# Kernel tuning notes

Measured on AMD Instinct MI355X. Metric: run time of the kernel, lower is better.

Reference implementation:

```python
import jax, jax.numpy as jnp
import numpy as np

NEG = -1e30  # safe 'log zero' for fp32 (avoids -inf NaNs in grads)


def _ctc_loss(logits, targets, input_lengths, target_lengths):
    """PyTorch-semantics CTC loss: blank=0, reduction='mean', zero_infinity=True.
    logits: [B,T,C] (pre-log-softmax), targets: [B,S] padded, lengths: [B].
    """
    B, T, C = logits.shape
    S = targets.shape[1]
    L = 2 * S + 1  # extended target length (blanks interleaved)
    logp = jax.nn.log_softmax(logits, axis=-1)  # [B,T,C]

    # extended targets: blank, y1, blank, y2, ..., blank
    ext = jnp.zeros((B, L), jnp.int32).at[:, 1::2].set(targets.astype(jnp.int32))
    lp_ext = jnp.take_along_axis(
        logp, jnp.broadcast_to(ext[:, None, :], (B, T, L)), axis=2)  # [B,T,L]

    pos = jnp.arange(L)
    ext_m2 = jnp.pad(ext, ((0, 0), (2, 0)))[:, :L]
    can_skip = (ext != 0) & (ext != ext_m2) & (pos >= 2)  # [B,L]

    def shift(a, k):
        return jnp.pad(a, ((0, 0), (k, 0)), constant_values=NEG)[:, :L]

    def lse3(a, b, c):
        m = jnp.maximum(jnp.maximum(a, b), c)
        return m + jnp.log(jnp.exp(a - m) + jnp.exp(b - m) + jnp.exp(c - m))

    alpha0 = (jnp.full((B, L), NEG, logits.dtype)
              .at[:, 0].set(lp_ext[:, 0, 0])
              .at[:, 1].set(lp_ext[:, 0, 1]))

    def step(alpha, xs):
        lp_t, t = xs  # lp_t: [B,L]
        a2 = shift(alpha, 1)
        a3 = jnp.where(can_skip, shift(alpha, 2), NEG)
        new = lp_t + lse3(alpha, a2, a3)
        # freeze alpha once past each sample's input_length
        alpha = jnp.where((t < input_lengths)[:, None], new, alpha)
        return alpha, None

    lp_T = jnp.swapaxes(lp_ext, 0, 1)  # [T,B,L]
    alpha, _ = jax.lax.scan(step, alpha0, (lp_T[1:], jnp.arange(1, T)))

    i1 = (2 * target_lengths - 1).astype(jnp.int32)
    i2 = (2 * target_lengths).astype(jnp.int32)
    a_last = jnp.take_along_axis(alpha, i1[:, None], axis=1)[:, 0]
    a_blank = jnp.take_along_axis(alpha, i2[:, None], axis=1)[:, 0]
    loss = -jnp.logaddexp(a_last, a_blank)  # [B]
    loss = jnp.where(loss > 1e29, 0.0, loss)  # zero_infinity=True
    return jnp.mean(loss / target_lengths.astype(loss.dtype))


def setup_inputs() -> dict:
    key = jax.random.key(0)
    ks = jax.random.split(key, 8)
    B, T = 32, 2000
    C_err, S_err = 4, 50
    C_ph, S_ph = 64, 200
    error_logits = jax.random.normal(ks[0], (B, T, C_err), jnp.float32)
    phoneme_logits = jax.random.normal(ks[1], (B, T, C_ph), jnp.float32)
    # labels in [1, C): blank=0 never appears in targets
    error_targets = jax.random.randint(ks[2], (B, S_err), 1, C_err, jnp.int32)
    phoneme_targets = jax.random.randint(ks[3], (B, S_ph), 1, C_ph, jnp.int32)
    error_input_lengths = jax.random.randint(ks[4], (B,), T - T // 4, T + 1, jnp.int32)
    phoneme_input_lengths = jax.random.randint(ks[5], (B,), T - T // 4, T + 1, jnp.int32)
    error_target_lengths = jax.random.randint(ks[6], (B,), S_err // 2, S_err + 1, jnp.int32)
    phoneme_target_lengths = jax.random.randint(ks[7], (B,), S_ph // 2, S_ph + 1, jnp.int32)
    return {
        "error_logits": error_logits,
        "phoneme_logits": phoneme_logits,
        "error_targets": error_targets,
        "phoneme_targets": phoneme_targets,
        "error_input_lengths": error_input_lengths,
        "phoneme_input_lengths": phoneme_input_lengths,
        "error_target_lengths": error_target_lengths,
        "phoneme_target_lengths": phoneme_target_lengths,
    }


def reference(error_logits, phoneme_logits, error_targets, phoneme_targets,
              error_input_lengths, phoneme_input_lengths,
              error_target_lengths, phoneme_target_lengths):
    error_weight = 1.0
    phoneme_weight = 1.0
    error_loss = _ctc_loss(error_logits, error_targets,
                           error_input_lengths, error_target_lengths)
    phoneme_loss = _ctc_loss(phoneme_logits, phoneme_targets,
                             phoneme_input_lengths, phoneme_target_lengths)
    total_loss = error_weight * error_loss + phoneme_weight * phoneme_loss
    return total_loss
```

## Files before the change

kernel.cpp:

```cpp
#include <hip/hip_runtime.h>
#include <math.h>


static constexpr float  LOG2E = 1.4426950408889634f;
static constexpr double LN2D  = 0.6931471805599453;
static constexpr int GROWS = 2032;

#define DPP_WAVE_SHR1   0x138
#define DPP_ROW_SHR(n)  (0x110 | (n))
#define DPP_ROW_BCAST15 0x142
#define DPP_ROW_BCAST31 0x143

__device__ __forceinline__ float fexp2(float x) {
  return __builtin_amdgcn_exp2f(x);
}
__device__ __forceinline__ float flog2(float x) {
  return __builtin_amdgcn_logf(x);
}

__device__ __forceinline__ double dpp_shr1_f64(double x) {
  int lo = __double2loint(x), hi = __double2hiint(x);
  lo = __builtin_amdgcn_update_dpp(0, lo, DPP_WAVE_SHR1, 0xf, 0xf, true);
  hi = __builtin_amdgcn_update_dpp(0, hi, DPP_WAVE_SHR1, 0xf, 0xf, true);
  return __hiloint2double(hi, lo);
}

__device__ __forceinline__ int imax2(int a, int b) { return a > b ? a : b; }

__device__ __forceinline__ int wave_imax(int v) {
  v = imax2(v, __builtin_amdgcn_update_dpp(0, v, DPP_ROW_SHR(1), 0xf, 0xf, true));
  v = imax2(v, __builtin_amdgcn_update_dpp(0, v, DPP_ROW_SHR(2), 0xf, 0xf, true));
  v = imax2(v, __builtin_amdgcn_update_dpp(0, v, DPP_ROW_SHR(4), 0xf, 0xf, true));
  v = imax2(v, __builtin_amdgcn_update_dpp(0, v, DPP_ROW_SHR(8), 0xf, 0xf, true));
  v = imax2(v, __builtin_amdgcn_update_dpp(0, v, DPP_ROW_BCAST15, 0xf, 0xf, true));
  v = imax2(v, __builtin_amdgcn_update_dpp(0, v, DPP_ROW_BCAST31, 0xf, 0xf, true));
  return __builtin_amdgcn_readlane(v, 63);
}

template <int SZ>
__device__ __forceinline__ void dma(const float* g, float* l) {
  auto gp = (const __attribute__((address_space(1))) void*)g;
  auto lp = (__attribute__((address_space(3))) void*)l;
  if constexpr (SZ == 4) {
    __builtin_amdgcn_global_load_lds(gp, lp, 4, 0, 0);
  } else {
    __builtin_amdgcn_global_load_lds(gp, lp, 16, 0, 0);
  }
}

__device__ __forceinline__ void wait_vmcnt16() {
  __builtin_amdgcn_sched_barrier(0);
  __builtin_amdgcn_s_waitcnt(20336);
  __builtin_amdgcn_sched_barrier(0);
}
__device__ __forceinline__ void wait_vmcnt0() {
  __builtin_amdgcn_sched_barrier(0);
  __builtin_amdgcn_s_waitcnt(3952);
  __builtin_amdgcn_sched_barrier(0);
}


__global__ __launch_bounds__(256) void gather_all_kernel(
    const float* __restrict__ ph_logits, const float* __restrict__ err_logits,
    const int* __restrict__ ph_tgt, const int* __restrict__ err_tgt,
    float* __restrict__ Gph, float* __restrict__ Ger,
    float* __restrict__ Lpb_ph, float* __restrict__ Lpb_er) {
  const int lane = threadIdx.x & 63;
  const int t = blockIdx.x * 4 + (threadIdx.x >> 6);
  const int b = blockIdx.y;
  if (blockIdx.z == 0) {
    const float z = ph_logits[((size_t)b * 2000 + t) * 64 + lane] * LOG2E;
    float m = z;
#pragma unroll
    for (int off = 32; off >= 1; off >>= 1) m = fmaxf(m, __shfl_xor(m, off, 64));
    const float zm = z - m;
    const float e = fexp2(zm);
    float s = e;
#pragma unroll
    for (int off = 32; off >= 1; off >>= 1) s += __shfl_xor(s, off, 64);
    const int ei = __float_as_int(e);
    const float e0 = __int_as_float(__builtin_amdgcn_readlane(ei, 0));
    const float inv0 = 1.0f / e0;
    const int* tb = ph_tgt + b * 200;
    float o[4];
#pragma unroll
    for (int k = 0; k < 4; ++k) {
      const int si = lane * 4 + k;
      const int cls = (si < 200) ? tb[si] : 0;
      const float v = __int_as_float(__builtin_amdgcn_ds_bpermute(cls << 2, ei));
      o[k] = (si < 200) ? (v * inv0) : 0.0f;
    }
    *(float4*)(Gph + ((size_t)b * GROWS + t) * 256 + lane * 4) =
        make_float4(o[0], o[1], o[2], o[3]);
    if (lane == 0)
      Lpb_ph[(size_t)b * GROWS + t] = zm - flog2(s);
  } else {
    const float4 v = *(const float4*)(err_logits + ((size_t)b * 2000 + t) * 4);
    const float z0 = v.x * LOG2E, z1 = v.y * LOG2E, z2 = v.z * LOG2E,
                z3 = v.w * LOG2E;
    const float m = fmaxf(fmaxf(z0, z1), fmaxf(z2, z3));
    const float e0 = fexp2(z0 - m), e1 = fexp2(z1 - m);
    const float e2 = fexp2(z2 - m), e3 = fexp2(z3 - m);
    const int c1 = err_tgt[b * 50 + (lane < 50 ? lane : 49)];
    const float num = (c1 == 1) ? e1 : (c1 == 2) ? e2 : e3;
    Ger[((size_t)b * GROWS + t) * 64 + lane] = (lane < 50) ? (num / e0) : 0.0f;
    if (lane == 0)
      Lpb_er[(size_t)b * GROWS + t] = (z0 - m) - flog2(e0 + e1 + e2 + e3);
  }
}

template <int P> struct RowP { float v[P]; };

template <int P>
__device__ __forceinline__ RowP<P> load_rowp(const float* p) {
  RowP<P> r;
  if constexpr (P == 4) {
    const float4 a = *(const float4*)p;
    r.v[0] = a.x; r.v[1] = a.y; r.v[2] = a.z; r.v[3] = a.w;
  } else {
    r.v[0] = *p;
  }
  return r;
}

template <int P>
__device__ __forceinline__ void bl_renorm(double (&B)[P], double (&L)[P],
                                          int& K) {
  double mm = B[0];
#pragma unroll
  for (int k = 0; k < P; ++k) mm = fmax(fmax(mm, B[k]), L[k]);
  const int ex = (__double2hiint(mm) >> 20) & 0x7ff;
  const int emax = wave_imax(ex);
  if (emax > 0) {
    int d = 1523 - emax;
    if (d > 1023) d = 1023;
    if (d < -1022) d = -1022;
    const double sc = __hiloint2double((d + 1023) << 20, 0);
#pragma unroll
    for (int k = 0; k < P; ++k) { B[k] *= sc; L[k] *= sc; }
    K += d;
  }
}

template <int P>
__device__ __forceinline__ void bl_step(double (&B)[P], double (&L)[P],
                                        const double (&skipm)[P],
                                        const RowP<P>& f) {
  const double Lm1 = dpp_shr1_f64(L[P - 1]);
  double nB[P], nL[P];
#pragma unroll
  for (int k = 0; k < P; ++k) {
    const double Lp = (k >= 1) ? L[k - 1] : Lm1;
    nB[k] = B[k] + Lp;
    nL[k] = (double)f.v[k] * fma(skipm[k], Lp, B[k] + L[k]);
  }
#pragma unroll
  for (int k = 0; k < P; ++k) { B[k] = nB[k]; L[k] = nL[k]; }
}

template <int P, int S>
__device__ __forceinline__ void chain_bl3(
    const float* __restrict__ Glab,
    const float* __restrict__ Lpb,
    const int* __restrict__ tb, int len, int tl,
    float* __restrict__ out, double* sa, float* stage) {
  constexpr int LSTRIDE = 64 * P;
  const int lane = threadIdx.x;

  float spb = 0.f;
  for (int t = lane; t < len; t += 64) spb += Lpb[t];
#pragma unroll
  for (int off = 32; off >= 1; off >>= 1) spb += __shfl_xor(spb, off, 64);

  double skipm[P];
#pragma unroll
  for (int k = 0; k < P; ++k) {
    const int s = lane * P + k;
    skipm[k] = (s >= 1 && s < S && tb[s] != tb[s - 1]) ? 1.0 : 0.0;
  }

  double B[P], L[P];
#pragma unroll
  for (int k = 0; k < P; ++k) { B[k] = 0.0; L[k] = 0.0; }
  {
    const float r0 = Glab[0];
    if (lane == 0) { B[0] = 1.0; L[0] = (double)r0; }
  }
  int K = 0;

  const int ngroups = (len - 1) / 16;
  auto issue_group = [&](int g, int buf) {
    const float* rb = Glab + (size_t)(1 + g * 16) * LSTRIDE + lane * P;
    float* lb = stage + (size_t)buf * 16 * LSTRIDE;
#pragma unroll
    for (int u = 0; u < 16; ++u)
      dma<P * 4>(rb + u * LSTRIDE, lb + u * LSTRIDE);
  };

  if (ngroups >= 1) issue_group(0, 0);
  if (ngroups >= 2) issue_group(1, 1);

  for (int g = 0; g < ngroups; ++g) {
    if (g + 1 < ngroups) wait_vmcnt16();
    else                 wait_vmcnt0();
    bl_renorm<P>(B, L, K);
    const float* lb = stage + (size_t)(g & 1) * 16 * LSTRIDE + lane * P;
    RowP<P> c0 = load_rowp<P>(lb);
    RowP<P> c1 = load_rowp<P>(lb + LSTRIDE);
#pragma unroll
    for (int u = 0; u < 16; ++u) {
      RowP<P> c2 = c1;
      if (u + 2 < 16) c2 = load_rowp<P>(lb + (u + 2) * LSTRIDE);
      bl_step<P>(B, L, skipm, c0);
      c0 = c1; c1 = c2;
    }
    if (g + 2 < ngroups) issue_group(g + 2, g & 1);
  }
  for (int t = 1 + ngroups * 16; t < len; ++t) {
    if (((t - 1) & 15) == 0) bl_renorm<P>(B, L, K);
    const RowP<P> f = load_rowp<P>(Glab + (size_t)t * LSTRIDE + lane * P);
    bl_step<P>(B, L, skipm, f);
  }

  double* saB = sa;
  double* saL = sa + 64 * P;
#pragma unroll
  for (int k = 0; k < P; ++k) {
    saB[lane * P + k] = B[k];
    saL[lane * P + k] = L[k];
  }
  __syncthreads();
  if (lane == 0) {
    const double a = saL[tl - 1] + saB[tl];
    float loss = (float)((double)K * LN2D - log(a) - (double)spb * LN2D);
    if (!(loss < 1e29f)) loss = 0.f;
    atomicAdd(out, loss / ((float)tl * 32.0f));
  }
}

__global__ __launch_bounds__(64) void ctc_chains_dma_kernel(
    const float* __restrict__ Gph, const float* __restrict__ Ger,
    const float* __restrict__ Lpb_ph, const float* __restrict__ Lpb_er,
    const int* __restrict__ err_tgt, const int* __restrict__ ph_tgt,
    const int* __restrict__ err_il, const int* __restrict__ ph_il,
    const int* __restrict__ err_tl, const int* __restrict__ ph_tl,
    float* __restrict__ out) {
  __shared__ float stage[2 * 16 * 256];
  __shared__ double sa[512];
  const int blk = blockIdx.x;
  if (blk < 32) {
    int len = err_il[blk]; if (len > 2000) len = 2000;
    chain_bl3<1, 50>(Ger + (size_t)blk * GROWS * 64,
                     Lpb_er + (size_t)blk * GROWS, err_tgt + blk * 50, len,
                     err_tl[blk], out, sa, stage);
  } else {
    const int b = blk - 32;
    int len = ph_il[b]; if (len > 2000) len = 2000;
    chain_bl3<4, 200>(Gph + (size_t)b * GROWS * 256,
                      Lpb_ph + (size_t)b * GROWS, ph_tgt + b * 200, len,
                      ph_tl[b], out, sa, stage);
  }
}


__global__ __launch_bounds__(256) void softmax4_kernel(
    const float* __restrict__ x, float* __restrict__ p, int nrows) {
  int r = blockIdx.x * blockDim.x + threadIdx.x;
  if (r >= nrows) return;
  float4 v = *reinterpret_cast<const float4*>(x + (size_t)r * 4);
  float z0 = v.x * LOG2E, z1 = v.y * LOG2E, z2 = v.z * LOG2E, z3 = v.w * LOG2E;
  float m = fmaxf(fmaxf(z0, z1), fmaxf(z2, z3));
  float e0 = fexp2(z0 - m), e1 = fexp2(z1 - m);
  float e2 = fexp2(z2 - m), e3 = fexp2(z3 - m);
  float inv = 1.0f / (e0 + e1 + e2 + e3);
  float4 o;
  o.x = e0 * inv; o.y = e1 * inv; o.z = e2 * inv; o.w = e3 * inv;
  *reinterpret_cast<float4*>(p + (size_t)r * 4) = o;
}

__global__ __launch_bounds__(256) void softmax64_kernel(
    const float* __restrict__ x, float* __restrict__ p, int nrows) {
  int row = blockIdx.x * 4 + (threadIdx.x >> 6);
  int lane = threadIdx.x & 63;
  if (row >= nrows) return;
  float z = x[(size_t)row * 64 + lane] * LOG2E;
  float m = z;
#pragma unroll
  for (int off = 32; off >= 1; off >>= 1) m = fmaxf(m, __shfl_xor(m, off, 64));
  float e = fexp2(z - m);
  float s = e;
#pragma unroll
  for (int off = 32; off >= 1; off >>= 1) s += __shfl_xor(s, off, 64);
  p[(size_t)row * 64 + lane] = e * (1.0f / s);
}

template <int C, int S, int R>
__device__ __forceinline__ void ctc_chain_lin_fb(
    const float* __restrict__ p_b, const int* __restrict__ tgt_b,
    int len, int tl, float* __restrict__ out, double* sa) {
  constexpr int L = 2 * S + 1;
  const int lane = threadIdx.x;
  int idx[R];
  double skipm[R];
#pragma unroll
  for (int j = 0; j < R; ++j) {
    const int l = lane * R + j;
    int cls = 0;
    bool sk = false;
    if (l & 1) {
      const int s = (l - 1) >> 1;
      const int sc = (s < S) ? s : (S - 1);
      cls = tgt_b[sc];
      if (s >= 1 && s < S) sk = (cls != tgt_b[s - 1]);
    }
    idx[j] = cls * 4;
    skipm[j] = sk ? 1.0 : 0.0;
  }
  double alpha[R];
#pragma unroll
  for (int j = 0; j < R; ++j) {
    const int l = lane * R + j;
    alpha[j] = (l <= 1) ? (double)p_b[idx[j] >> 2] : 0.0;
  }
  int K = 0;
  const int cl = lane & (C - 1);
  float rv = p_b[(size_t)((1 < len - 1) ? 1 : (len - 1)) * C + cl];
  float pf[R];
#pragma unroll
  for (int j = 0; j < R; ++j)
    pf[j] = __int_as_float(__builtin_amdgcn_ds_bpermute(idx[j], __float_as_int(rv)));
  rv = p_b[(size_t)((2 < len - 1) ? 2 : (len - 1)) * C + cl];
  for (int t = 1; t < len; ++t) {
    if ((t & 31) == 0) {
      double m = alpha[0];
#pragma unroll
      for (int j = 1; j < R; ++j) m = fmax(m, alpha[j]);
#pragma unroll
      for (int off = 1; off < 64; off <<= 1) m = fmax(m, __shfl_xor(m, off, 64));
      const long long bits = __double_as_longlong(m);
      const int e = (int)((bits >> 52) & 0x7FF);
      if (e > 0) {
        const double sc = __longlong_as_double((long long)(2046 - e) << 52);
#pragma unroll
        for (int j = 0; j < R; ++j) alpha[j] *= sc;
        K += 1023 - e;
      }
    }
    const int tn = (t + 2 < len) ? (t + 2) : (len - 1);
    const float rvn = p_b[(size_t)tn * C + cl];
    float pfn[R];
#pragma unroll
    for (int j = 0; j < R; ++j)
      pfn[j] = __int_as_float(__builtin_amdgcn_ds_bpermute(idx[j], __float_as_int(rv)));
    double am1 = __shfl_up(alpha[R - 1], 1, 64);
    double am2 = __shfl_up(alpha[R - 2], 1, 64);
    if (lane == 0) { am1 = 0.0; am2 = 0.0; }
    double na[R];
#pragma unroll
    for (int j = 0; j < R; ++j) {
      const double a0 = alpha[j];
      const double a1 = (j >= 1) ? alpha[j - 1] : am1;
      const double a2 = (j >= 2) ? alpha[j - 2] : ((j == 1) ? am1 : am2);
      double s = a0 + a1;
      s = fma(skipm[j], a2, s);
      na[j] = (double)pf[j] * s;
    }
#pragma unroll
    for (int j = 0; j < R; ++j) alpha[j] = na[j];
#pragma unroll
    for (int j = 0; j < R; ++j) pf[j] = pfn[j];
    rv = rvn;
  }
#pragma unroll
  for (int j = 0; j < R; ++j) {
    const int l = lane * R + j;
    if (l < L) sa[l] = alpha[j];
  }
  __syncthreads();
  if (lane == 0) {
    const double a = sa[2 * tl - 1] + sa[2 * tl];
    float loss = (float)((double)K * LN2D - log(a));
    if (!(loss < 1e29f)) loss = 0.0f;
    atomicAdd(out, loss / ((float)tl * 32.0f));
  }
}

__global__ __launch_bounds__(64) void ctc_chains_fb_kernel(
    const float* __restrict__ p_err, const float* __restrict__ p_ph,
    const int* __restrict__ err_tgt, const int* __restrict__ ph_tgt,
    const int* __restrict__ err_il, const int* __restrict__ ph_il,
    const int* __restrict__ err_tl, const int* __restrict__ ph_tl,
    float* __restrict__ out) {
  __shared__ double sa[512];
  const int T = 2000;
  const int blk = blockIdx.x;
  if (blk < 32) {
    const int b = blk;
    int len = err_il[b]; if (len > T) len = T;
    ctc_chain_lin_fb<4, 50, 2>(p_err + (size_t)b * T * 4, err_tgt + b * 50, len,
                               err_tl[b], out, sa);
  } else {
    const int b = blk - 32;
    int len = ph_il[b]; if (len > T) len = T;
    ctc_chain_lin_fb<64, 200, 7>(p_ph + (size_t)b * T * 64, ph_tgt + b * 200,
                                 len, ph_tl[b], out, sa);
  }
}


extern "C" void kernel_launch(void* const* d_in, const int* in_sizes, int n_in,
                              void* d_out, int out_size, void* d_ws,
                              size_t ws_size, hipStream_t stream) {
  const float* err_logits = (const float*)d_in[0];
  const float* ph_logits  = (const float*)d_in[1];
  const int* err_tgt = (const int*)d_in[2];
  const int* ph_tgt  = (const int*)d_in[3];
  const int* err_il  = (const int*)d_in[4];
  const int* ph_il   = (const int*)d_in[5];
  const int* err_tl  = (const int*)d_in[6];
  const int* ph_tl   = (const int*)d_in[7];
  float* out = (float*)d_out;

  const size_t gph = (size_t)32 * GROWS * 256;
  const size_t ger = (size_t)32 * GROWS * 64;
  const size_t lpb = (size_t)32 * GROWS;
  const size_t need = (gph + ger + 2 * lpb) * sizeof(float);

  (void)hipMemsetAsync(d_out, 0, sizeof(float), stream);

  if (ws_size >= need) {
    float* Gph = (float*)d_ws;
    float* Ger = Gph + gph;
    float* Lpb_ph = Ger + ger;
    float* Lpb_er = Lpb_ph + lpb;
    dim3 grid(500, 32, 2);
    gather_all_kernel<<<grid, 256, 0, stream>>>(ph_logits, err_logits, ph_tgt,
                                                err_tgt, Gph, Ger, Lpb_ph,
                                                Lpb_er);
    ctc_chains_dma_kernel<<<64, 64, 0, stream>>>(Gph, Ger, Lpb_ph, Lpb_er,
                                                 err_tgt, ph_tgt, err_il,
                                                 ph_il, err_tl, ph_tl, out);
  } else {
    const int B = 32, T = 2000;
    const int rows = B * T;
    float* p_err = (float*)d_ws;
    float* p_ph  = p_err + (size_t)rows * 4;
    softmax4_kernel<<<(rows + 255) / 256, 256, 0, stream>>>(err_logits, p_err, rows);
    softmax64_kernel<<<(rows + 3) / 4, 256, 0, stream>>>(ph_logits, p_ph, rows);
    ctc_chains_fb_kernel<<<64, 64, 0, stream>>>(p_err, p_ph, err_tgt, ph_tgt,
                                                err_il, ph_il, err_tl, ph_tl, out);
  }
}
```

Baseline: 231.1 us.

## Replace LDS DMA staging with register double-buffered prefetch in CTC chain

The serial CTC recurrence kernel previously staged 16-row groups of gathered probabilities into LDS via global_load_lds with manual vmcnt waits. It now keeps two 16-row register buffers per lane and issues the global loads for group g+2 while stepping through group g, and it handles the remaining tail rows with a batched 15-row register load. The blank-logprob sum loop is also unrolled by 8 to increase memory-level parallelism. This removes LDS round-trips and explicit waits from the latency-bound chain, but raises register pressure (32×P floats for the buffers) and relies on the compiler's waitcnt placement, which may stall early.

```diff
diff --git a/kernel.cpp b/kernel.cpp
--- a/kernel.cpp
+++ b/kernel.cpp
@@ -35,28 +35,6 @@
   v = imax2(v, __builtin_amdgcn_update_dpp(0, v, DPP_ROW_BCAST15, 0xf, 0xf, true));
   v = imax2(v, __builtin_amdgcn_update_dpp(0, v, DPP_ROW_BCAST31, 0xf, 0xf, true));
   return __builtin_amdgcn_readlane(v, 63);
-}
-
-template <int SZ>
-__device__ __forceinline__ void dma(const float* g, float* l) {
-  auto gp = (const __attribute__((address_space(1))) void*)g;
-  auto lp = (__attribute__((address_space(3))) void*)l;
-  if constexpr (SZ == 4) {
-    __builtin_amdgcn_global_load_lds(gp, lp, 4, 0, 0);
-  } else {
-    __builtin_amdgcn_global_load_lds(gp, lp, 16, 0, 0);
-  }
-}
-
-__device__ __forceinline__ void wait_vmcnt16() {
-  __builtin_amdgcn_sched_barrier(0);
-  __builtin_amdgcn_s_waitcnt(20336);
-  __builtin_amdgcn_sched_barrier(0);
-}
-__device__ __forceinline__ void wait_vmcnt0() {
-  __builtin_amdgcn_sched_barrier(0);
-  __builtin_amdgcn_s_waitcnt(3952);
-  __builtin_amdgcn_sched_barrier(0);
 }
 
 
@@ -159,16 +137,24 @@
 }
 
 template <int P, int S>
-__device__ __forceinline__ void chain_bl3(
+__device__ __forceinline__ void chain_bl4(
     const float* __restrict__ Glab,
     const float* __restrict__ Lpb,
     const int* __restrict__ tb, int len, int tl,
-    float* __restrict__ out, double* sa, float* stage) {
+    float* __restrict__ out, double* sa) {
   constexpr int LSTRIDE = 64 * P;
   const int lane = threadIdx.x;
 
   float spb = 0.f;
-  for (int t = lane; t < len; t += 64) spb += Lpb[t];
+  for (int t0 = lane; t0 < len; t0 += 512) {
+#pragma unroll
+    for (int u = 0; u < 8; ++u) {
+      const int t = t0 + u * 64;
+      const int tc = (t < len) ? t : 0;
+      const float v = Lpb[tc];
+      spb += (t < len) ? v : 0.0f;
+    }
+  }
 #pragma unroll
   for (int off = 32; off >= 1; off >>= 1) spb += __shfl_xor(spb, off, 64);
 
@@ -188,38 +174,70 @@
   }
   int K = 0;
 
+  const float* gp = Glab + lane * P;
   const int ngroups = (len - 1) / 16;
-  auto issue_group = [&](int g, int buf) {
-    const float* rb = Glab + (size_t)(1 + g * 16) * LSTRIDE + lane * P;
-    float* lb = stage + (size_t)buf * 16 * LSTRIDE;
+
+  RowP<P> bufA[16], bufB[16];
+  if (ngroups >= 1) {
+    const float* rb = gp + (size_t)1 * LSTRIDE;
 #pragma unroll
     for (int u = 0; u < 16; ++u)
-      dma<P * 4>(rb + u * LSTRIDE, lb + u * LSTRIDE);
-  };
-
-  if (ngroups >= 1) issue_group(0, 0);
-  if (ngroups >= 2) issue_group(1, 1);
-
-  for (int g = 0; g < ngroups; ++g) {
-    if (g + 1 < ngroups) wait_vmcnt16();
-    else                 wait_vmcnt0();
+      bufA[u] = load_rowp<P>(rb + (size_t)u * LSTRIDE);
+  }
+  if (ngroups >= 2) {
+    const float* rb = gp + (size_t)17 * LSTRIDE;
+#pragma unroll
+    for (int u = 0; u < 16; ++u)
+      bufB[u] = load_rowp<P>(rb + (size_t)u * LSTRIDE);
+  }
+
+  int g = 0;
+  for (; g + 2 <= ngroups; g += 2) {
+    {
+      bl_renorm<P>(B, L, K);
+      const int gn = (g + 2 < ngroups) ? (g + 2) : 0;
+      const float* nx = gp + (size_t)(1 + gn * 16) * LSTRIDE;
+#pragma unroll
+      for (int u = 0; u < 16; ++u) {
+        bl_step<P>(B, L, skipm, bufA[u]);
+        bufA[u] = load_rowp<P>(nx + (size_t)u * LSTRIDE);
+      }
+    }
+    {
+      bl_renorm<P>(B, L, K);
+      const int gn = (g + 3 < ngroups) ? (g + 3) : 0;
+      const float* nx = gp + (size_t)(1 + gn * 16) * LSTRIDE;
+#pragma unroll
+      for (int u = 0; u < 16; ++u) {
+        bl_step<P>(B, L, skipm, bufB[u]);
+        bufB[u] = load_rowp<P>(nx + (size_t)u * LSTRIDE);
+      }
+    }
+  }
+  if (g < ngroups) {
     bl_renorm<P>(B, L, K);
-    const float* lb = stage + (size_t)(g & 1) * 16 * LSTRIDE + lane * P;
-    RowP<P> c0 = load_rowp<P>(lb);
-    RowP<P> c1 = load_rowp<P>(lb + LSTRIDE);
-#pragma unroll
-    for (int u = 0; u < 16; ++u) {
-      RowP<P> c2 = c1;
-      if (u + 2 < 16) c2 = load_rowp<P>(lb + (u + 2) * LSTRIDE);
-      bl_step<P>(B, L, skipm, c0);
-      c0 = c1; c1 = c2;
-    }
-    if (g + 2 < ngroups) issue_group(g + 2, g & 1);
-  }
-  for (int t = 1 + ngroups * 16; t < len; ++t) {
-    if (((t - 1) & 15) == 0) bl_renorm<P>(B, L, K);
-    const RowP<P> f = load_rowp<P>(Glab + (size_t)t * LSTRIDE + lane * P);
-    bl_step<P>(B, L, skipm, f);
+#pragma unroll
+    for (int u = 0; u < 16; ++u) bl_step<P>(B, L, skipm, bufA[u]);
+    ++g;
+  }
+
+  {
+    const int tstart = 1 + ngroups * 16;
+    RowP<P> bufT[15];
+#pragma unroll
+    for (int u = 0; u < 15; ++u) {
+      int t = tstart + u;
+      if (t > len - 1) t = len - 1;
+      bufT[u] = load_rowp<P>(gp + (size_t)t * LSTRIDE);
+    }
+#pragma unroll
+    for (int u = 0; u < 15; ++u) {
+      const int t = tstart + u;
+      if (t < len) {
+        if (u == 0) bl_renorm<P>(B, L, K);
+        bl_step<P>(B, L, skipm, bufT[u]);
+      }
+    }
   }
 
   double* saB = sa;
@@ -238,27 +256,26 @@
   }
 }
 
-__global__ __launch_bounds__(64) void ctc_chains_dma_kernel(
+__global__ __launch_bounds__(64) void ctc_chains_reg_kernel(
     const float* __restrict__ Gph, const float* __restrict__ Ger,
     const float* __restrict__ Lpb_ph, const float* __restrict__ Lpb_er,
     const int* __restrict__ err_tgt, const int* __restrict__ ph_tgt,
     const int* __restrict__ err_il, const int* __restrict__ ph_il,
     const int* __restrict__ err_tl, const int* __restrict__ ph_tl,
     float* __restrict__ out) {
-  __shared__ float stage[2 * 16 * 256];
   __shared__ double sa[512];
   const int blk = blockIdx.x;
   if (blk < 32) {
     int len = err_il[blk]; if (len > 2000) len = 2000;
-    chain_bl3<1, 50>(Ger + (size_t)blk * GROWS * 64,
+    chain_bl4<1, 50>(Ger + (size_t)blk * GROWS * 64,
                      Lpb_er + (size_t)blk * GROWS, err_tgt + blk * 50, len,
-                     err_tl[blk], out, sa, stage);
+                     err_tl[blk], out, sa);
   } else {
     const int b = blk - 32;
     int len = ph_il[b]; if (len > 2000) len = 2000;
-    chain_bl3<4, 200>(Gph + (size_t)b * GROWS * 256,
+    chain_bl4<4, 200>(Gph + (size_t)b * GROWS * 256,
                       Lpb_ph + (size_t)b * GROWS, ph_tgt + b * 200, len,
-                      ph_tl[b], out, sa, stage);
+                      ph_tl[b], out, sa);
   }
 }
 
@@ -437,7 +454,7 @@
     gather_all_kernel<<<grid, 256, 0, stream>>>(ph_logits, err_logits, ph_tgt,
                                                 err_tgt, Gph, Ger, Lpb_ph,
                                                 Lpb_er);
-    ctc_chains_dma_kernel<<<64, 64, 0, stream>>>(Gph, Ger, Lpb_ph, Lpb_er,
+    ctc_chains_reg_kernel<<<64, 64, 0, stream>>>(Gph, Ger, Lpb_ph, Lpb_er,
                                                  err_tgt, ph_tgt, err_il,
                                                  ph_il, err_tl, ph_tl, out);
   } else {
```

After: 204.1 us. -11.7%, faster.
